# Optimization experiments

Hardware: AMD Instinct MI355X
Metric: run time of the kernel (lower is better)

Reference implementation:

```python
import jax, jax.numpy as jnp
import numpy as np

NEG = -1e30  # finite stand-in for -inf to keep gradients NaN-free


def setup_inputs() -> dict:
    key = jax.random.key(0)
    k1, k2, k3 = jax.random.split(key, 3)
    T, B, V, L = 1600, 48, 1000, 128
    # acoustic model output: already log-softmax normalized, layout [T, B, V]
    logits = jax.random.normal(k1, (T, B, V), dtype=jnp.float32)
    log_probs = jax.nn.log_softmax(logits, axis=-1)
    # flat concatenated targets (nonzero labels; 0 is blank), uniform length L per utt
    targets = jax.random.randint(k2, (B * L,), 1, V, dtype=jnp.int32)
    input_lengths = jax.random.randint(k3, (B,), 3 * T // 4, T + 1, dtype=jnp.int32)
    target_lengths = jnp.full((B,), L, dtype=jnp.int32)
    return {
        "log_probs": log_probs,
        "targets": targets,
        "input_lengths": input_lengths,
        "target_lengths": target_lengths,
    }


def _ctc_neg_log_likelihood(log_probs, targets, input_lengths, target_lengths):
    """Exact log-semiring CTC forward (total score over all alignments),
    equivalent to k2.intersect_dense(ctc_topo o linear_fsa, dense) +
    get_tot_scores(log_semiring=True). Returns -sum_b log p(y_b | x_b).
    log_probs: [T, B, V]; targets: flat [B*L]; lengths: [B].
    """
    T, B, V = log_probs.shape
    L = targets.shape[0] // B
    tg = targets.reshape(B, L)
    S = 2 * L + 1  # blank-interleaved extended label sequence

    ext = jnp.zeros((B, S), dtype=jnp.int32).at[:, 1::2].set(tg)  # [B, S]
    # skip transition s-2 -> s allowed iff label[s] != blank and != label[s-2]
    allow_skip = jnp.concatenate(
        [jnp.zeros((B, 2), dtype=bool),
         (ext[:, 2:] != 0) & (ext[:, 2:] != ext[:, :-2])],
        axis=1,
    )

    def emit(lp_t):  # [B, V] -> [B, S]
        return jnp.take_along_axis(lp_t, ext, axis=1)

    e0 = emit(log_probs[0])
    alpha0 = jnp.full((B, S), NEG, dtype=log_probs.dtype)
    alpha0 = alpha0.at[:, 0].set(e0[:, 0]).at[:, 1].set(e0[:, 1])

    def step(alpha, xs):
        lp_t, t = xs
        prev1 = jnp.pad(alpha[:, :-1], ((0, 0), (1, 0)), constant_values=NEG)
        prev2 = jnp.pad(alpha[:, :-2], ((0, 0), (2, 0)), constant_values=NEG)
        a = jnp.logaddexp(alpha, prev1)
        a = jnp.where(allow_skip, jnp.logaddexp(a, prev2), a)
        new = a + emit(lp_t)
        # freeze alpha once past each utterance's input length
        alpha = jnp.where((t < input_lengths)[:, None], new, alpha)
        return alpha, None

    alpha, _ = jax.lax.scan(step, alpha0, (log_probs[1:], jnp.arange(1, T)))

    # all target_lengths are L, so the final states are S-1 (last blank) and S-2
    tot_scores = jnp.logaddexp(alpha[:, S - 1], alpha[:, S - 2])  # [B]
    return -jnp.sum(tot_scores)


def reference(log_probs, targets, input_lengths, target_lengths):
    return _ctc_neg_log_likelihood(log_probs, targets, input_lengths, target_lengths)
```

## Files before the change

kernel.cpp:

```cpp
#include <hip/hip_runtime.h>
#include <math.h>

#define TT 1600
#define BB 48
#define VV 1000
#define LL 128
#define EMS 132
#define EMTOT (TT*EMS)
#define TILE 60
#define TILEF (TILE*EMS)
#define NTILES 27

#define DPPF(x, ctrl) __int_as_float(__builtin_amdgcn_update_dpp( \
    0, __float_as_int(x), (ctrl), 0xf, 0xf, true))

typedef const __attribute__((address_space(1))) unsigned int* gldlds_src_t;
typedef __attribute__((address_space(3))) unsigned int*       gldlds_dst_t;

__global__ __launch_bounds__(256) void ctc_gather_kernel(
    const float* __restrict__ lp,
    const int* __restrict__ targets,
    float* __restrict__ em)
{
  __shared__ float rb[8000];
  const int tid  = threadIdx.x;
  const int wv   = tid >> 6;
  const int lane = tid & 63;
  const size_t row0 = (size_t)blockIdx.x * 8;

  const float4* src = (const float4*)(lp + row0 * VV);
#pragma unroll
  for (int i = 0; i < 8; i++) {
    int idx = tid + (i << 8);
    if (idx < 2000)
      __builtin_amdgcn_global_load_lds(
          (gldlds_src_t)(src + idx),
          (gldlds_dst_t)(rb + ((size_t)((i << 8) + (wv << 6)) << 2)),
          16, 0, 0);
  }
  __syncthreads();

  const int t  = (int)(row0 / BB);
  const int b0 = (int)(row0 % BB);
#pragma unroll
  for (int r = 0; r < 2; r++) {
    const int bl = 2 * wv + r;
    const int b  = b0 + bl;
    const int* __restrict__ tg = targets + b * LL;
    const float* row = rb + bl * 1000;
    const int g0 = (lane == 0) ? 0 : tg[lane - 1];
    const int g1 = tg[lane + 63];
    float v0 = row[g0];
    float v1 = row[g1];
    float* erow = em + (size_t)b * EMTOT + (size_t)t * EMS;
    erow[(lane == 0) ? 0 : (lane + 1)] = __expf(v0);
    erow[lane + 65] = __expf(v1);
    if (lane == 0) erow[129] = __expf(row[tg[127]]);
  }
}

__global__ __launch_bounds__(256) void ctc_dp_kernel(
    const float* __restrict__ em,
    const int* __restrict__ targets,
    const int* __restrict__ input_lengths,
    float* __restrict__ out)
{
  __shared__ float sbuf[2][TILEF];
  const int b    = blockIdx.x;
  const int lane = threadIdx.x & 63;
  const int wv   = threadIdx.x >> 6;
  const int NS   = input_lengths[b] - 1;
  const float* __restrict__ base = em + (size_t)b * EMTOT;

  float skip1 = 0.f, skip3 = 0.f, m63 = 0.f, sel1648 = 0.f, sel32 = 0.f;
  if (wv == 0) {
    const int* __restrict__ tg = targets + b * LL;
    const int c0  = tg[2 * lane];
    const int c1  = tg[2 * lane + 1];
    const int cm1 = (lane > 0) ? tg[2 * lane - 1] : c0;
    skip1   = (lane > 0 && c0 != cm1) ? 1.0f : 0.0f;
    skip3   = (c1 != c0) ? 1.0f : 0.0f;
    m63     = (lane == 63) ? 1.0f : 0.0f;
    sel1648 = (lane == 16 || lane == 48) ? 1.0f : 0.0f;
    sel32   = (lane == 32) ? 1.0f : 0.0f;
  }

  float a0 = 0.f, a1 = 0.f, a2 = 0.f, a3 = 0.f, a4 = 0.f;
  int esum = 0;
  float sc_p = 1.0f;
  int   se_p = 0;
  float  pb_r[4];
  float2 ev_r[4];

#define STAGE(KN) do {                                               \
    const float4* src_ = (const float4*)(base + (size_t)(KN) * TILEF); \
    float* dst_ = sbuf[(KN) & 1];                                    \
    const int nf4_ = ((KN) == NTILES - 1) ? 1320 : 1980;             \
    for (int j = wv - 1; j < 31; j += 3) {                           \
      int idx_ = (j << 6) + lane;                                    \
      if (idx_ < nf4_)                                               \
        __builtin_amdgcn_global_load_lds(                            \
            (gldlds_src_t)(src_ + idx_),                             \
            (gldlds_dst_t)(dst_ + (j << 8)), 16, 0, 0);              \
    }                                                                \
  } while (0)

#define STEP(PB, EV) do {                                            \
    float am1 = DPPF(a3, 0x111);                                     \
    float h15 = DPPF(a3, 0x142);                                     \
    float h31 = DPPF(a3, 0x143);                                     \
    am1 = fmaf(sel1648, h15, am1);                                   \
    am1 = fmaf(sel32,   h31, am1);                                   \
    float s0 = a0 + am1;                                             \
    float s1 = fmaf(skip1, am1, a0 + a1);                            \
    float s2 = a1 + a2;                                              \
    float s3 = fmaf(skip3, a1, a2 + a3);                             \
    float s4 = fmaf(a3, m63, a4);                                    \
    a0 = s0 * (PB); a1 = s1 * (EV).x; a2 = s2 * (PB);                \
    a3 = s3 * (EV).y; a4 = s4 * (PB);                                \
  } while (0)

#define RESCALE_DEFERRED() do {                                      \
    a0 *= sc_p; a1 *= sc_p; a2 *= sc_p; a3 *= sc_p; a4 *= sc_p;      \
    esum -= se_p;                                                    \
    float mx = fmaxf(fmaxf(fmaxf(a0, a1), fmaxf(a2, a3)), a4);       \
    mx = fmaxf(mx, DPPF(mx, 0x111));                                 \
    mx = fmaxf(mx, DPPF(mx, 0x112));                                 \
    mx = fmaxf(mx, DPPF(mx, 0x114));                                 \
    mx = fmaxf(mx, DPPF(mx, 0x118));                                 \
    mx = fmaxf(mx, DPPF(mx, 0x142));                                 \
    mx = fmaxf(mx, DPPF(mx, 0x143));          \
    int eb = (__builtin_amdgcn_readlane(__float_as_int(mx), 63) >> 23) & 0xFF; \
    int se = 157 - eb;                         \
    se = se < -126 ? -126 : (se > 127 ? 127 : se);                   \
    sc_p = __uint_as_float((unsigned)(se + 127) << 23);              \
    se_p = se;                                                       \
  } while (0)

  if (wv) STAGE(0);
  __syncthreads();

  for (int k = 0; k < NTILES; k++) {
    if (wv) {
      if (k + 1 < NTILES) STAGE(k + 1);
    } else {
      const float* lb = sbuf[k & 1];
      if (k == 0 && lane == 0) { a0 = lb[0]; a1 = lb[2]; }
      int tbeg = (k == 0) ? 1 : k * TILE;
      int tend = k * TILE + TILE - 1;
      if (tend > NS) tend = NS;
      int n = tend - tbeg + 1;
      if (n > 0) {
        const float* lb0 = lb + (tbeg - k * TILE) * EMS;
        const float* lbe = lb0 + 2 + 2 * lane;
#define LOADSLOT(D, TF) do {                                         \
    int off_ = (TF) * EMS;                                           \
    pb_r[D] = lb0[off_];                                             \
    ev_r[D] = *(const float2*)(lbe + off_);                          \
  } while (0)
#pragma unroll
        for (int d = 0; d < 4; d++) { if (d < n) LOADSLOT(d, d); }
        int i = 0;
        while (i + 4 <= n) {
#pragma unroll
          for (int d = 0; d < 4; d++) {
            STEP(pb_r[d], ev_r[d]);
            int tf = i + 4 + d;
            if (tf < n) LOADSLOT(d, tf);
          }
          RESCALE_DEFERRED();
          i += 4;
        }
#pragma unroll
        for (int d = 0; d < 3; d++) {
          if (i + d < n) STEP(pb_r[d], ev_r[d]);
        }
#undef LOADSLOT
      }
    }
    __syncthreads();
  }

  if (wv == 0 && lane == 63) {
    a3 *= sc_p; a4 *= sc_p; esum -= se_p;
    float tot = __logf(a3 + a4) + (float)esum * 0.69314718055994530942f;
    atomicAdd(out, -tot);
  }
#undef STEP
#undef RESCALE_DEFERRED
#undef STAGE
}

extern "C" void kernel_launch(void* const* d_in, const int* in_sizes, int n_in,
                              void* d_out, int out_size, void* d_ws, size_t ws_size,
                              hipStream_t stream) {
  const float* lp            = (const float*)d_in[0];
  const int*   targets       = (const int*)d_in[1];
  const int*   input_lengths = (const int*)d_in[2];

  float* em  = (float*)d_ws;
  float* out = (float*)d_out;

  hipMemsetAsync(out, 0, sizeof(float), stream);

  ctc_gather_kernel<<<(TT * BB) / 8, 256, 0, stream>>>(lp, targets, em);
  ctc_dp_kernel<<<BB, 256, 0, stream>>>(em, targets, input_lengths, out);
}
```

Baseline: 559.0 us.

## Store label emissions as fp16 with 1024x prescale and split blank emissions

The gathered emission probabilities for the 128 labels are now stored as packed fp16 pairs in a [T, B, 64] layout. Each value is prescaled by 1024 to keep fp16 precision, and the total is corrected for the scale afterwards. Blank emissions go to a separate fp32 array that is loaded once into LDS, and the DP tile grows to 100 timesteps. This halves the intermediate buffer traffic between the gather and DP kernels and cuts the number of tile stages. The cost is fp16 rounding and subnormal/underflow risk on the emission values, plus strided per-timestep loads in the DP staging.

```diff
diff --git a/kernel.cpp b/kernel.cpp
--- a/kernel.cpp
+++ b/kernel.cpp
@@ -1,15 +1,15 @@
 #include <hip/hip_runtime.h>
+#include <hip/hip_fp16.h>
 #include <math.h>
 
 #define TT 1600
 #define BB 48
 #define VV 1000
 #define LL 128
-#define EMS 132
-#define EMTOT (TT*EMS)
-#define TILE 60
-#define TILEF (TILE*EMS)
-#define NTILES 27
+#define TILE 100
+#define NTILES 16
+#define TILEU (TILE * 64)
+#define LN1024 6.93147180559945309f
 
 #define DPPF(x, ctrl) __int_as_float(__builtin_amdgcn_update_dpp( \
     0, __float_as_int(x), (ctrl), 0xf, 0xf, true))
@@ -20,7 +20,8 @@
 __global__ __launch_bounds__(256) void ctc_gather_kernel(
     const float* __restrict__ lp,
     const int* __restrict__ targets,
-    float* __restrict__ em)
+    __half* __restrict__ emL,
+    float* __restrict__ emB)
 {
   __shared__ float rb[8000];
   const int tid  = threadIdx.x;
@@ -46,31 +47,28 @@
   for (int r = 0; r < 2; r++) {
     const int bl = 2 * wv + r;
     const int b  = b0 + bl;
-    const int* __restrict__ tg = targets + b * LL;
+    const int2 g = ((const int2*)(targets + b * LL))[lane];
     const float* row = rb + bl * 1000;
-    const int g0 = (lane == 0) ? 0 : tg[lane - 1];
-    const int g1 = tg[lane + 63];
-    float v0 = row[g0];
-    float v1 = row[g1];
-    float* erow = em + (size_t)b * EMTOT + (size_t)t * EMS;
-    erow[(lane == 0) ? 0 : (lane + 1)] = __expf(v0);
-    erow[lane + 65] = __expf(v1);
-    if (lane == 0) erow[129] = __expf(row[tg[127]]);
+    float e0 = __expf(row[g.x] + LN1024);
+    float e1 = __expf(row[g.y] + LN1024);
+    ((__half2*)emL)[(size_t)(t * BB + b) * 64 + lane] = __floats2half2_rn(e0, e1);
+    if (lane == 0) emB[b * TT + t] = __expf(row[0] + LN1024);
   }
 }
 
 __global__ __launch_bounds__(256) void ctc_dp_kernel(
-    const float* __restrict__ em,
+    const __half* __restrict__ emL,
+    const float* __restrict__ emB,
     const int* __restrict__ targets,
     const int* __restrict__ input_lengths,
     float* __restrict__ out)
 {
-  __shared__ float sbuf[2][TILEF];
+  __shared__ unsigned int sbuf[2][TILEU];
+  __shared__ float pbbuf[TT];
   const int b    = blockIdx.x;
   const int lane = threadIdx.x & 63;
   const int wv   = threadIdx.x >> 6;
   const int NS   = input_lengths[b] - 1;
-  const float* __restrict__ base = em + (size_t)b * EMTOT;
 
   float skip1 = 0.f, skip3 = 0.f, m63 = 0.f, sel1648 = 0.f, sel32 = 0.f;
   if (wv == 0) {
@@ -92,17 +90,16 @@
   float  pb_r[4];
   float2 ev_r[4];
 
-#define STAGE(KN) do {                                               \
-    const float4* src_ = (const float4*)(base + (size_t)(KN) * TILEF); \
-    float* dst_ = sbuf[(KN) & 1];                                    \
-    const int nf4_ = ((KN) == NTILES - 1) ? 1320 : 1980;             \
-    for (int j = wv - 1; j < 31; j += 3) {                           \
-      int idx_ = (j << 6) + lane;                                    \
-      if (idx_ < nf4_)                                               \
-        __builtin_amdgcn_global_load_lds(                            \
-            (gldlds_src_t)(src_ + idx_),                             \
-            (gldlds_dst_t)(dst_ + (j << 8)), 16, 0, 0);              \
-    }                                                                \
+#define STAGE(KN) do {                                                 \
+    const char* srcb_ = (const char*)emL + ((size_t)(KN) * TILE * BB + b) * 256; \
+    unsigned int* dst_ = sbuf[(KN) & 1];                               \
+    for (int j = wv - 1; j < 25; j += 3) {                             \
+      int idx_ = (j << 6) + lane;                                      \
+      __builtin_amdgcn_global_load_lds(                                \
+          (gldlds_src_t)(srcb_ + (size_t)(idx_ >> 4) * (BB * 256)      \
+                               + ((idx_ & 15) << 4)),                  \
+          (gldlds_dst_t)(dst_ + (idx_ << 2)), 16, 0, 0);               \
+    }                                                                  \
   } while (0)
 
 #define STEP(PB, EV) do {                                            \
@@ -137,26 +134,38 @@
     se_p = se;                                                       \
   } while (0)
 
-  if (wv) STAGE(0);
+  if (wv) {
+    for (int j = wv - 1; j < 7; j += 3) {
+      int idx = (j << 6) + lane;
+      if (idx < 400)
+        __builtin_amdgcn_global_load_lds(
+            (gldlds_src_t)(emB + (size_t)b * TT + ((size_t)idx << 2)),
+            (gldlds_dst_t)(pbbuf + (idx << 2)), 16, 0, 0);
+    }
+    STAGE(0);
+  }
   __syncthreads();
 
   for (int k = 0; k < NTILES; k++) {
     if (wv) {
       if (k + 1 < NTILES) STAGE(k + 1);
     } else {
-      const float* lb = sbuf[k & 1];
-      if (k == 0 && lane == 0) { a0 = lb[0]; a1 = lb[2]; }
+      const unsigned int* tb = sbuf[k & 1];
+      if (k == 0 && lane == 0) {
+        a0 = pbbuf[0];
+        unsigned int u0 = tb[0];
+        a1 = __half22float2(*reinterpret_cast<const __half2*>(&u0)).x;
+      }
       int tbeg = (k == 0) ? 1 : k * TILE;
       int tend = k * TILE + TILE - 1;
       if (tend > NS) tend = NS;
       int n = tend - tbeg + 1;
       if (n > 0) {
-        const float* lb0 = lb + (tbeg - k * TILE) * EMS;
-        const float* lbe = lb0 + 2 + 2 * lane;
+        const unsigned int* lb0 = tb + (tbeg - k * TILE) * 64 + lane;
 #define LOADSLOT(D, TF) do {                                         \
-    int off_ = (TF) * EMS;                                           \
-    pb_r[D] = lb0[off_];                                             \
-    ev_r[D] = *(const float2*)(lbe + off_);                          \
+    pb_r[D] = pbbuf[tbeg + (TF)];              \
+    unsigned int u_ = lb0[(TF) * 64];         \
+    ev_r[D] = __half22float2(*reinterpret_cast<const __half2*>(&u_)); \
   } while (0)
 #pragma unroll
         for (int d = 0; d < 4; d++) { if (d < n) LOADSLOT(d, d); }
@@ -183,7 +192,8 @@
 
   if (wv == 0 && lane == 63) {
     a3 *= sc_p; a4 *= sc_p; esum -= se_p;
-    float tot = __logf(a3 + a4) + (float)esum * 0.69314718055994530942f;
+    float tot = __logf(a3 + a4)
+              + ((float)esum - 10.0f * (float)(NS + 1)) * 0.69314718055994530942f;
     atomicAdd(out, -tot);
   }
 #undef STEP
@@ -198,11 +208,12 @@
   const int*   targets       = (const int*)d_in[1];
   const int*   input_lengths = (const int*)d_in[2];
 
-  float* em  = (float*)d_ws;
-  float* out = (float*)d_out;
+  float*  emB = (float*)d_ws;
+  __half* emL = (__half*)((char*)d_ws + 307200);
+  float*  out = (float*)d_out;
 
   hipMemsetAsync(out, 0, sizeof(float), stream);
 
-  ctc_gather_kernel<<<(TT * BB) / 8, 256, 0, stream>>>(lp, targets, em);
-  ctc_dp_kernel<<<BB, 256, 0, stream>>>(em, targets, input_lengths, out);
+  ctc_gather_kernel<<<(TT * BB) / 8, 256, 0, stream>>>(lp, targets, emL, emB);
+  ctc_dp_kernel<<<BB, 256, 0, stream>>>(emL, emB, targets, input_lengths, out);
 }
```

New measurement: 561.6 us. Within noise of the previous version (+0.5%).
